# Kernel optimization log

Measured on AMD Instinct MI355X. Metric: run time of the kernel, lower is better.

Reference implementation:

```python
import jax, jax.numpy as jnp
import numpy as np

DIM = 1024
NUM_HEADS = 8
HEAD_DIM = 128
MAX_SEQ_LEN = 2048
ATTN_SCALE = 0.12
RMS_EPS = 1.1920929e-07  # torch float32 eps (F.rms_norm default)


def rms_norm(x):
    return x * jax.lax.rsqrt(jnp.mean(jnp.square(x), axis=-1, keepdims=True) + RMS_EPS)


def rope_tables(T):
    # angular_freq: (1/1024)**linspace(0,1,head_dim//4), padded with head_dim//4 zeros -> length head_dim//2
    af = (1.0 / 1024.0) ** np.linspace(0.0, 1.0, HEAD_DIM // 4, dtype=np.float32)
    af = np.concatenate([af, np.zeros(HEAD_DIM // 4, dtype=np.float32)])
    t = np.arange(T, dtype=np.float32)
    theta = np.einsum('i,j->ij', t, af)  # [T, head_dim//2]
    return jnp.asarray(np.cos(theta)), jnp.asarray(np.sin(theta))


def apply_rope(x_BTHD, cos, sin):
    # cos/sin: [T, head_dim//2] -> broadcast [1,T,1,hd//2]
    c = cos[None, :, None, :]
    s = sin[None, :, None, :]
    x1, x2 = jnp.split(x_BTHD, 2, axis=-1)
    y1 = x1 * c + x2 * s
    y2 = -x1 * s + x2 * c
    return jnp.concatenate([y1, y2], axis=-1)


def setup_inputs() -> dict:
    key = jax.random.key(0)
    k1, k2, k3, k4, k5 = jax.random.split(key, 5)
    B, T = 4, 2048
    hdim = NUM_HEADS * HEAD_DIM
    std = 0.5 * DIM ** (-0.5)
    bound = (3.0 ** 0.5) * std
    x = jax.random.normal(k1, (B, T, DIM), dtype=jnp.float32)
    ve = jax.random.normal(k2, (B, T, DIM), dtype=jnp.float32)
    sa_lambdas = jax.random.uniform(k3, (2,), dtype=jnp.float32)
    qkv_w = jax.random.uniform(k4, (3, hdim, DIM), dtype=jnp.float32, minval=-bound, maxval=bound)
    # original inits c_proj to zeros; use small random so the output is non-trivial
    c_proj_weight = jax.random.normal(k5, (DIM, hdim), dtype=jnp.float32) * 0.02
    return {"x": x, "ve": ve, "sa_lambdas": sa_lambdas, "qkv_w": qkv_w,
            "c_proj_weight": c_proj_weight}


def reference(x, ve, sa_lambdas, qkv_w, c_proj_weight):
    B, T, D = x.shape
    H, hd = NUM_HEADS, HEAD_DIM
    Wqkv = qkv_w.reshape(3 * H * hd, D)
    qkv = jnp.einsum('btd,ed->bte', x, Wqkv).reshape(B, T, 3 * H, hd)
    q, k, v = jnp.split(qkv, 3, axis=-2)  # each [B,T,H,hd]
    q, k = rms_norm(q), rms_norm(k)
    cos, sin = rope_tables(T)
    q, k = apply_rope(q, cos, sin), apply_rope(k, cos, sin)
    v = sa_lambdas[0] * v + sa_lambdas[1] * ve.reshape(B, T, H, hd)
    # [B,H,T,T] scores
    attn = jnp.einsum('bqhd,bkhd->bhqk', q, k) * ATTN_SCALE
    causal = jnp.triu(jnp.ones((T, T), dtype=bool), k=1)
    attn = jnp.where(causal[None, None], -jnp.inf, attn)
    attn = jax.nn.softmax(attn, axis=-1)
    y = jnp.einsum('bhqk,bkhd->bqhd', attn, v).reshape(B, T, H * hd)
    return jnp.einsum('bte,de->btd', y, c_proj_weight)
```

## Files before the change

kernel.cpp:

```cpp
#include <hip/hip_runtime.h>

#define DIM 1024
#define NH 8
#define HD 128
#define T_SEQ 2048
#define NTOK 8192
#define QKV_N 3072
#define ATTN_SCALE 0.12f
#define RMS_EPS 1.1920929e-07f

using f32x4  = __attribute__((ext_vector_type(4))) float;
using bf16x8 = __attribute__((ext_vector_type(8))) __bf16;

__device__ __forceinline__ unsigned short f2bf(float f) {
    unsigned int u = __builtin_bit_cast(unsigned int, f);
    u += 0x7fffu + ((u >> 16) & 1u);
    return (unsigned short)(u >> 16);
}
__device__ __forceinline__ float bf2f(unsigned short s) {
    unsigned int u = ((unsigned int)s) << 16;
    return __builtin_bit_cast(float, u);
}

__device__ __forceinline__ void gll16(const void* g, void* l) {
    __builtin_amdgcn_global_load_lds(
        (const __attribute__((address_space(1))) unsigned int*)g,
        (__attribute__((address_space(3))) unsigned int*)l, 16, 0, 0);
}

#define VMCNT(n) asm volatile("s_waitcnt vmcnt(" #n ")" ::: "memory")

__global__ __launch_bounds__(256) void cvt_f32_bf16(const float* __restrict__ in,
                                                    unsigned short* __restrict__ out,
                                                    int n4) {
    int i = blockIdx.x * 256 + threadIdx.x;
    if (i < n4) {
        float4 f = ((const float4*)in)[i];
        ushort4 o;
        o.x = f2bf(f.x); o.y = f2bf(f.y); o.z = f2bf(f.z); o.w = f2bf(f.w);
        ((ushort4*)out)[i] = o;
    }
}

#define GBM 256
#define GBN 128
#define GBK 64
#define SLOT_A 32768
#define SLOT_SZ 49152

template<int OUTF32>
__global__ __launch_bounds__(512, 1) void gemm256(const unsigned short* __restrict__ A,
                                                  const unsigned short* __restrict__ B,
                                                  void* __restrict__ Cout,
                                                  int M, int N, int K, int nbn) {
    __shared__ __align__(16) char smem[147456];
    const int tid  = threadIdx.x;
    const int lane = tid & 63;
    const int w    = tid >> 6;
    const int wm   = w >> 1, wn = w & 1;
    const int lr   = lane & 15, lg = lane >> 4;
    const int xsw  = (lr & 7) << 3;

    const int chunk = gridDim.x >> 3;
    const int bid2  = (blockIdx.x & 7) * chunk + (blockIdx.x >> 3);
    const int m0 = (bid2 / nbn) * GBM;
    const int n0 = (bid2 % nbn) * GBN;

    const int rsub = lane >> 3;
    const int csw  = ((lane & 7) ^ rsub) << 3;

    char* s0 = smem;
    char* s1 = smem + SLOT_SZ;
    char* s2 = smem + 2*SLOT_SZ;

    auto stage = [&](int kt, char* slot) {
        const int kb = kt * GBK;
        #pragma unroll
        for (int i = 0; i < 4; ++i) {
            int c = w*4 + i;
            gll16(&A[(size_t)(m0 + c*8 + rsub)*K + kb + csw], slot + c*1024);
        }
        #pragma unroll
        for (int i = 0; i < 2; ++i) {
            int c = w*2 + i;
            gll16(&B[(size_t)(n0 + c*8 + rsub)*K + kb + csw], slot + SLOT_A + c*1024);
        }
    };

    f32x4 acc[4][4] = {};
    const int KT = K / GBK;

    stage(0, s0);
    stage(1, s1);
    VMCNT(6);
    __builtin_amdgcn_s_barrier();
    __builtin_amdgcn_sched_barrier(0);

    for (int t = 0; t < KT; ++t) {
        if (t + 2 < KT) stage(t + 2, s2);
        const unsigned short* sA = (const unsigned short*)s0;
        const unsigned short* sB = (const unsigned short*)(s0 + SLOT_A);
        bf16x8 bfr[4][2];
        #pragma unroll
        for (int n = 0; n < 4; ++n)
            #pragma unroll
            for (int kk = 0; kk < 2; ++kk)
                bfr[n][kk] = *(const bf16x8*)&sB[(wn*64 + n*16 + lr)*64 + ((kk*32 + lg*8) ^ xsw)];
        #pragma unroll
        for (int m = 0; m < 4; ++m) {
            bf16x8 af[2];
            #pragma unroll
            for (int kk = 0; kk < 2; ++kk)
                af[kk] = *(const bf16x8*)&sA[(wm*64 + m*16 + lr)*64 + ((kk*32 + lg*8) ^ xsw)];
            __builtin_amdgcn_s_setprio(1);
            #pragma unroll
            for (int n = 0; n < 4; ++n)
                #pragma unroll
                for (int kk = 0; kk < 2; ++kk)
                    acc[m][n] = __builtin_amdgcn_mfma_f32_16x16x32_bf16(af[kk], bfr[n][kk], acc[m][n], 0, 0, 0);
            __builtin_amdgcn_s_setprio(0);
        }
        if (t + 2 < KT) { VMCNT(6); }
        else            { VMCNT(0); }
        __builtin_amdgcn_s_barrier();
        __builtin_amdgcn_sched_barrier(0);
        char* tmp = s0; s0 = s1; s1 = s2; s2 = tmp;
    }

    __syncthreads();
    float* sc = (float*)(smem + (size_t)w * 17408);
    #pragma unroll
    for (int m = 0; m < 4; ++m)
        #pragma unroll
        for (int n = 0; n < 4; ++n)
            #pragma unroll
            for (int r = 0; r < 4; ++r)
                sc[(m*16 + lg*4 + r)*68 + n*16 + lr] = acc[m][n][r];

    if (OUTF32) {
        float* C = (float*)Cout;
        #pragma unroll
        for (int rnd = 0; rnd < 16; ++rnd) {
            int g = rnd*64 + lane;
            int row = g >> 4, c4 = (g & 15) * 4;
            float4 v = *(float4*)&sc[row*68 + c4];
            *(float4*)&C[(size_t)(m0 + wm*64 + row)*N + n0 + wn*64 + c4] = v;
        }
    } else {
        unsigned short* C = (unsigned short*)Cout;
        #pragma unroll
        for (int rnd = 0; rnd < 8; ++rnd) {
            int g = rnd*64 + lane;
            int row = g >> 3, c8 = (g & 7) * 8;
            float4 v0 = *(float4*)&sc[row*68 + c8];
            float4 v1 = *(float4*)&sc[row*68 + c8 + 4];
            uint4 o;
            o.x = f2bf(v0.x) | ((unsigned)f2bf(v0.y) << 16);
            o.y = f2bf(v0.z) | ((unsigned)f2bf(v0.w) << 16);
            o.z = f2bf(v1.x) | ((unsigned)f2bf(v1.y) << 16);
            o.w = f2bf(v1.z) | ((unsigned)f2bf(v1.w) << 16);
            *(uint4*)&C[(size_t)(m0 + wm*64 + row)*N + n0 + wn*64 + c8] = o;
        }
    }
}

__global__ __launch_bounds__(256) void qkv_post(const unsigned short* __restrict__ qkv,
                                                unsigned short* __restrict__ qO,
                                                unsigned short* __restrict__ kO) {
    int gw   = (blockIdx.x * 256 + threadIdx.x) >> 6;
    int lane = threadIdx.x & 63;
    int h     = gw & 7;
    int token = gw >> 3;
    int t     = token & (T_SEQ-1);
    int b     = token >> 11;

    const unsigned short* base = qkv + (size_t)token * QKV_N + h*HD;
    float q1 = bf2f(base[lane]),        q2 = bf2f(base[lane+64]);
    float k1 = bf2f(base[1024+lane]),   k2 = bf2f(base[1024+lane+64]);

    float sq = q1*q1 + q2*q2;
    float sk = k1*k1 + k2*k2;
    #pragma unroll
    for (int m = 1; m < 64; m <<= 1) {
        sq += __shfl_xor(sq, m);
        sk += __shfl_xor(sk, m);
    }
    float qs = rsqrtf(sq * (1.0f/128.0f) + RMS_EPS) * ATTN_SCALE;
    float ks = rsqrtf(sk * (1.0f/128.0f) + RMS_EPS);
    q1 *= qs; q2 *= qs; k1 *= ks; k2 *= ks;

    float theta = (lane < 32) ? (float)t * exp2f((float)lane * (-10.0f/31.0f)) : 0.0f;
    float sn, cs;
    sincosf(theta, &sn, &cs);
    float qy1 =  q1*cs + q2*sn, qy2 = -q1*sn + q2*cs;
    float ky1 =  k1*cs + k2*sn, ky2 = -k1*sn + k2*cs;

    size_t obase = ((size_t)(b*NH + h) * T_SEQ + t) * HD;
    qO[obase + lane]      = f2bf(qy1);
    qO[obase + lane + 64] = f2bf(qy2);
    kO[obase + lane]      = f2bf(ky1);
    kO[obase + lane + 64] = f2bf(ky2);
}

__global__ __launch_bounds__(256) void vmix_t(const unsigned short* __restrict__ qkv,
                                              const float* __restrict__ ve,
                                              const float* __restrict__ lam,
                                              unsigned short* __restrict__ vt) {
    __shared__ unsigned short lT[128*72];
    const int tid = threadIdx.x;
    const int t0  = blockIdx.x * 64;
    const int bh  = blockIdx.y;
    const int b = bh >> 3, h = bh & 7;
    const float l0 = lam[0], l1 = lam[1];

    #pragma unroll
    for (int it = 0; it < 4; ++it) {
        int g  = it*256 + tid;
        int t  = g >> 4;
        int d8 = (g & 15) << 3;
        size_t token = (size_t)b*T_SEQ + t0 + t;
        ushort4 v0 = *(const ushort4*)&qkv[token*QKV_N + 2048 + h*HD + d8];
        ushort4 v1 = *(const ushort4*)&qkv[token*QKV_N + 2048 + h*HD + d8 + 4];
        float4 e0 = *(const float4*)&ve[token*DIM + h*HD + d8];
        float4 e1 = *(const float4*)&ve[token*DIM + h*HD + d8 + 4];
        lT[(d8+0)*72 + t] = f2bf(l0*bf2f(v0.x) + l1*e0.x);
        lT[(d8+1)*72 + t] = f2bf(l0*bf2f(v0.y) + l1*e0.y);
        lT[(d8+2)*72 + t] = f2bf(l0*bf2f(v0.z) + l1*e0.z);
        lT[(d8+3)*72 + t] = f2bf(l0*bf2f(v0.w) + l1*e0.w);
        lT[(d8+4)*72 + t] = f2bf(l0*bf2f(v1.x) + l1*e1.x);
        lT[(d8+5)*72 + t] = f2bf(l0*bf2f(v1.y) + l1*e1.y);
        lT[(d8+6)*72 + t] = f2bf(l0*bf2f(v1.z) + l1*e1.z);
        lT[(d8+7)*72 + t] = f2bf(l0*bf2f(v1.w) + l1*e1.w);
    }
    __syncthreads();
    #pragma unroll
    for (int it = 0; it < 4; ++it) {
        int g  = it*256 + tid;
        int d  = g >> 3;
        int t8 = (g & 7) << 3;
        uint4 pk = *(const uint4*)&lT[d*72 + t8];
        *(uint4*)&vt[((size_t)bh*HD + d)*T_SEQ + t0 + t8] = pk;
    }
}

__global__ __launch_bounds__(256) void attn_fwd(const unsigned short* __restrict__ Q,
                                                const unsigned short* __restrict__ K,
                                                const unsigned short* __restrict__ Vt,
                                                unsigned short* __restrict__ Y) {
    __shared__ unsigned short lK[2][64*128];
    __shared__ unsigned short lV[2][128*64];
    __shared__ unsigned short lP[4][16*64];

    const int tid  = threadIdx.x;
    const int lane = tid & 63;
    const int w    = tid >> 6;
    const int lr   = lane & 15, lg = lane >> 4;

    const int lin = blockIdx.y * 16 + blockIdx.x;
    const int bh  = (lin & 7)*4 + ((lin >> 3) & 3);
    const int p   = lin >> 5;
    const int qtA = p, qtB = 31 - p;

    const unsigned short* Qg = Q  + (size_t)bh * T_SEQ * HD;
    const unsigned short* Kg = K  + (size_t)bh * T_SEQ * HD;
    const unsigned short* Vg = Vt + (size_t)bh * HD * T_SEQ;
    const int q0A = qtA*64 + w*16;
    const int q0B = qtB*64 + w*16;

    auto stage = [&](int kt, int s) {
        const int kbase = kt * 64;
        #pragma unroll
        for (int i = 0; i < 4; ++i) {
            int c = w*4 + i;
            int row = c*4 + (lane >> 4);
            int col = ((lane & 15) << 3) ^ ((row & 7) << 3);
            gll16(&Kg[(size_t)(kbase + row)*HD + col], &lK[s][c*512]);
        }
        #pragma unroll
        for (int i = 0; i < 4; ++i) {
            int c = w*4 + i;
            int row = c*8 + (lane >> 3);
            int col = ((lane & 7) << 3) ^ ((row & 7) << 3);
            gll16(&Vg[(size_t)row*T_SEQ + kbase + col], &lV[s][c*512]);
        }
    };

    bf16x8 qfA[4], qfB[4];
    #pragma unroll
    for (int kk = 0; kk < 4; ++kk) {
        qfA[kk] = *(const bf16x8*)&Qg[(size_t)(q0A + lr)*HD + kk*32 + lg*8];
        qfB[kk] = *(const bf16x8*)&Qg[(size_t)(q0B + lr)*HD + kk*32 + lg*8];
    }
    VMCNT(0);
    #pragma unroll
    for (int kk = 0; kk < 4; ++kk)
        asm volatile("" :: "v"(qfA[kk]), "v"(qfB[kk]));

    f32x4 oA[8] = {}, oB[8] = {};
    float psA[4] = {0.f,0.f,0.f,0.f}, psB[4] = {0.f,0.f,0.f,0.f};

    auto pass = [&](const bf16x8* qf, f32x4* o, float* ps, int q0, bool diag,
                    int kbase, const unsigned short* lKc, const unsigned short* lVc) {
        f32x4 sf[4];
        #pragma unroll
        for (int j = 0; j < 4; ++j) {
            f32x4 s = {0.f,0.f,0.f,0.f};
            __builtin_amdgcn_s_setprio(1);
            #pragma unroll
            for (int kk = 0; kk < 4; ++kk) {
                bf16x8 kf = *(const bf16x8*)&lKc[(j*16+lr)*128 + ((kk*32 + lg*8) ^ ((lr&7)<<3))];
                s = __builtin_amdgcn_mfma_f32_16x16x32_bf16(qf[kk], kf, s, 0, 0, 0);
            }
            __builtin_amdgcn_s_setprio(0);
            sf[j] = s;
        }
        if (diag) {
            #pragma unroll
            for (int j = 0; j < 4; ++j)
                #pragma unroll
                for (int r = 0; r < 4; ++r) {
                    int kcol = kbase + j*16 + lr;
                    int qrow = q0 + lg*4 + r;
                    if (kcol > qrow) sf[j][r] = -INFINITY;
                }
        }
        #pragma unroll
        for (int j = 0; j < 4; ++j)
            #pragma unroll
            for (int r = 0; r < 4; ++r) {
                float pp = __expf(sf[j][r]);
                sf[j][r] = pp;
                ps[r] += pp;
            }
        #pragma unroll
        for (int j = 0; j < 4; ++j)
            #pragma unroll
            for (int r = 0; r < 4; ++r) {
                int prow = lg*4 + r;
                lP[w][prow*64 + ((j*16 + lr) ^ ((prow&7)<<3))] = f2bf(sf[j][r]);
            }
        asm volatile("" ::: "memory");
        bf16x8 pf[2];
        #pragma unroll
        for (int kk = 0; kk < 2; ++kk)
            pf[kk] = *(const bf16x8*)&lP[w][lr*64 + ((kk*32 + lg*8) ^ ((lr&7)<<3))];
        #pragma unroll
        for (int n = 0; n < 8; ++n) {
            __builtin_amdgcn_s_setprio(1);
            #pragma unroll
            for (int kk = 0; kk < 2; ++kk) {
                bf16x8 vf = *(const bf16x8*)&lVc[(n*16+lr)*64 + ((kk*32 + lg*8) ^ ((lr&7)<<3))];
                o[n] = __builtin_amdgcn_mfma_f32_16x16x32_bf16(pf[kk], vf, o[n], 0, 0, 0);
            }
            __builtin_amdgcn_s_setprio(0);
        }
    };

    stage(0, 0);
    for (int kt = 0; kt <= qtB; ++kt) {
        __builtin_amdgcn_s_barrier();
        const bool pre = (kt + 1 <= qtB);
        if (pre) stage(kt + 1, (kt + 1) & 1);
        if (pre) { VMCNT(8); }
        else     { VMCNT(0); }
        __builtin_amdgcn_sched_barrier(0);
        const int kbase = kt * 64;
        const unsigned short* lKc = lK[kt & 1];
        const unsigned short* lVc = lV[kt & 1];
        if (kt <= qtA) pass(qfA, oA, psA, q0A, kt == qtA, kbase, lKc, lVc);
        pass(qfB, oB, psB, q0B, kt == qtB, kbase, lKc, lVc);
    }

    #pragma unroll
    for (int m = 1; m < 16; m <<= 1)
        #pragma unroll
        for (int r = 0; r < 4; ++r) {
            psA[r] += __shfl_xor(psA[r], m);
            psB[r] += __shfl_xor(psB[r], m);
        }
    float riA[4], riB[4];
    #pragma unroll
    for (int r = 0; r < 4; ++r) { riA[r] = 1.0f / psA[r]; riB[r] = 1.0f / psB[r]; }

    const int b = bh >> 3, h = bh & 7;
    #pragma unroll
    for (int n = 0; n < 8; ++n)
        #pragma unroll
        for (int r = 0; r < 4; ++r) {
            int d = n*16 + lr;
            int qrowA = q0A + lg*4 + r;
            int qrowB = q0B + lg*4 + r;
            Y[((size_t)(b*T_SEQ + qrowA))*DIM + h*HD + d] = f2bf(oA[n][r] * riA[r]);
            Y[((size_t)(b*T_SEQ + qrowB))*DIM + h*HD + d] = f2bf(oB[n][r] * riB[r]);
        }
}

extern "C" void kernel_launch(void* const* d_in, const int* in_sizes, int n_in,
                              void* d_out, int out_size, void* d_ws, size_t ws_size,
                              hipStream_t stream) {
    const float* x      = (const float*)d_in[0];
    const float* ve     = (const float*)d_in[1];
    const float* lam    = (const float*)d_in[2];
    const float* qkvw   = (const float*)d_in[3];
    const float* cprojw = (const float*)d_in[4];

    char* ws = (char*)d_ws;
    unsigned short* xb  = (unsigned short*)(ws);
    unsigned short* wqb = (unsigned short*)(ws + 16777216);
    unsigned short* cpb = (unsigned short*)(ws + 23068672);
    unsigned short* qkv = (unsigned short*)(ws + 25165824);
    unsigned short* qa  = (unsigned short*)(ws + 75497472);
    unsigned short* ka  = (unsigned short*)(ws + 92274688);
    unsigned short* vt  = (unsigned short*)(ws + 109051904);
    unsigned short* ya  = (unsigned short*)(ws + 125829120);

    cvt_f32_bf16<<<8192, 256, 0, stream>>>(x, xb, 2097152);
    cvt_f32_bf16<<<3072, 256, 0, stream>>>(qkvw, wqb, 786432);
    cvt_f32_bf16<<<1024, 256, 0, stream>>>(cprojw, cpb, 262144);

    gemm256<0><<<768, 512, 0, stream>>>(xb, wqb, qkv, NTOK, QKV_N, DIM, 24);
    qkv_post<<<16384, 256, 0, stream>>>(qkv, qa, ka);
    vmix_t<<<dim3(32, 32), 256, 0, stream>>>(qkv, ve, lam, vt);
    attn_fwd<<<dim3(16, 32), 256, 0, stream>>>(qa, ka, vt, ya);
    gemm256<1><<<256, 512, 0, stream>>>(ya, cpb, (float*)d_out, NTOK, DIM, DIM, 8);
}
```

Baseline: 202.1 us.

## Add 256x256 eight-phase QKV GEMM, RoPE table, fused dual-tile attention pass

Adds a new 256x256-tile GEMM with an eight-wave phased schedule (split LDS halves, barriers between MFMA phases) for the QKV projection, which halves the grid and increases operand reuse per tile. The attention kernel now shares each K fragment and each V fragment between both query tiles in one combined pass, and switches to exp2 with log2e folded into the q scale. RoPE cos/sin are precomputed into a table in the workspace rather than computed with sincos per thread. Attention gets a launch bound hint of 2 blocks per CU. These trade higher register pressure and heavier barrier synchronisation for fewer LDS reads and less transcendental work.

```diff
diff --git a/kernel.cpp b/kernel.cpp
--- a/kernel.cpp
+++ b/kernel.cpp
@@ -29,6 +29,9 @@
 }
 
 #define VMCNT(n) asm volatile("s_waitcnt vmcnt(" #n ")" ::: "memory")
+#define LGKM0 do { asm volatile("s_waitcnt lgkmcnt(0)" ::: "memory"); \
+                   __builtin_amdgcn_sched_barrier(0); } while(0)
+#define PH_BAR __builtin_amdgcn_s_barrier()
 
 __global__ __launch_bounds__(256) void cvt_f32_bf16(const float* __restrict__ in,
                                                     unsigned short* __restrict__ out,
@@ -42,9 +45,189 @@
     }
 }
 
-#define GBM 256
-#define GBN 128
-#define GBK 64
+__global__ __launch_bounds__(256) void rope_tab(float2* __restrict__ tab) {
+    int idx = blockIdx.x * 256 + threadIdx.x;
+    int t = idx >> 5, i = idx & 31;
+    float th = (float)t * exp2f((float)i * (-10.0f/31.0f));
+    float sn, cs;
+    sincosf(th, &sn, &cs);
+    tab[idx] = make_float2(cs, sn);
+}
+
+template<int OUTF32>
+__global__ __launch_bounds__(512, 1) void gemm8p(const unsigned short* __restrict__ A,
+                                                 const unsigned short* __restrict__ B,
+                                                 void* __restrict__ Cout,
+                                                 int M, int N, int K, int nbn) {
+    __shared__ __align__(16) char smem[139264];
+    const int tid  = threadIdx.x;
+    const int lane = tid & 63;
+    const int w    = tid >> 6;
+    const int wm   = w >> 2, wn = w & 3;
+    const int lr   = lane & 15, lg = lane >> 4;
+
+    const int chunk = gridDim.x >> 3;
+    const int bid2  = (blockIdx.x & 7) * chunk + (blockIdx.x >> 3);
+    const int bm = (bid2 / nbn) * 256;
+    const int bn = (bid2 % nbn) * 256;
+
+    const int srow = lane >> 3;
+    const int scol = ((lane & 7) ^ srow) << 3;
+    const int KT = K / 64;
+
+    auto ldsA = [&](int p, int h) -> unsigned short* {
+        return (unsigned short*)(smem + p*65536 + h*16384);
+    };
+    auto ldsB = [&](int p, int h) -> unsigned short* {
+        return (unsigned short*)(smem + p*65536 + 32768 + h*16384);
+    };
+    auto stA = [&](int t, int p, int h) {
+        if (t >= KT) return;
+        char* dst = (char*)ldsA(p, h);
+        #pragma unroll
+        for (int i = 0; i < 2; ++i) {
+            int c = w*2 + i;
+            gll16(&A[(size_t)(bm + h*128 + c*8 + srow)*K + t*64 + scol], dst + c*1024);
+        }
+    };
+    auto stB = [&](int t, int p, int h) {
+        if (t >= KT) return;
+        char* dst = (char*)ldsB(p, h);
+        #pragma unroll
+        for (int i = 0; i < 2; ++i) {
+            int c = w*2 + i;
+            gll16(&B[(size_t)(bn + h*128 + c*8 + srow)*K + t*64 + scol], dst + c*1024);
+        }
+    };
+
+    f32x4 acc[8][4] = {};
+    bf16x8 a[4][2], b0[2][2], b1[2][2];
+
+    auto rdA4 = [&](int p, int qm) {
+        const unsigned short* base = ldsA(p, wm);
+        #pragma unroll
+        for (int m = 0; m < 4; ++m) {
+            int row = qm*64 + m*16 + lr;
+            int sw = (row & 7) << 3;
+            #pragma unroll
+            for (int kk = 0; kk < 2; ++kk)
+                a[m][kk] = *(const bf16x8*)&base[row*64 + ((kk*32 + lg*8) ^ sw)];
+        }
+    };
+    auto rdB2 = [&](int p, int qn, bf16x8 (*bq)[2]) {
+        const unsigned short* base = ldsB(p, wn >> 1);
+        #pragma unroll
+        for (int n = 0; n < 2; ++n) {
+            int row = (wn & 1)*64 + qn*32 + n*16 + lr;
+            int sw = (row & 7) << 3;
+            #pragma unroll
+            for (int kk = 0; kk < 2; ++kk)
+                bq[n][kk] = *(const bf16x8*)&base[row*64 + ((kk*32 + lg*8) ^ sw)];
+        }
+    };
+    auto mm = [&](int qm, int qn, bf16x8 (*bq)[2]) {
+        __builtin_amdgcn_s_setprio(1);
+        #pragma unroll
+        for (int m = 0; m < 4; ++m)
+            #pragma unroll
+            for (int n = 0; n < 2; ++n)
+                #pragma unroll
+                for (int kk = 0; kk < 2; ++kk)
+                    acc[qm*4+m][qn*2+n] =
+                        __builtin_amdgcn_mfma_f32_16x16x32_bf16(a[m][kk], bq[n][kk],
+                                                                acc[qm*4+m][qn*2+n], 0, 0, 0);
+        __builtin_amdgcn_s_setprio(0);
+    };
+
+    stB(0, 0, 0); stB(0, 0, 1); stA(0, 0, 0); stA(0, 0, 1);
+    stB(1, 1, 0); stB(1, 1, 1);
+    VMCNT(4);
+    PH_BAR;
+
+    for (int i = 0; i < KT/2; ++i) {
+        const int t0 = 2*i;
+        const bool steady = (i + 1 < KT/2);
+        rdA4(0, 0); rdB2(0, 0, b0);
+        stA(t0+1, 1, 0);
+        PH_BAR; LGKM0;
+        mm(0, 0, b0);
+        PH_BAR;
+        rdB2(0, 1, b1);
+        stA(t0+1, 1, 1);
+        PH_BAR; LGKM0;
+        mm(0, 1, b1);
+        PH_BAR;
+        rdA4(0, 1);
+        stB(t0+2, 0, 0);
+        PH_BAR; LGKM0;
+        mm(1, 0, b0);
+        PH_BAR;
+        stB(t0+2, 0, 1);
+        if (steady) { VMCNT(4); } else { VMCNT(0); }
+        PH_BAR;
+        mm(1, 1, b1);
+        PH_BAR;
+        rdA4(1, 0); rdB2(1, 0, b0);
+        stA(t0+2, 0, 0);
+        PH_BAR; LGKM0;
+        mm(0, 0, b0);
+        PH_BAR;
+        rdB2(1, 1, b1);
+        stA(t0+2, 0, 1);
+        PH_BAR; LGKM0;
+        mm(0, 1, b1);
+        PH_BAR;
+        rdA4(1, 1);
+        stB(t0+3, 1, 0);
+        PH_BAR; LGKM0;
+        mm(1, 0, b0);
+        PH_BAR;
+        stB(t0+3, 1, 1);
+        if (steady) { VMCNT(4); } else { VMCNT(0); }
+        PH_BAR;
+        mm(1, 1, b1);
+        PH_BAR;
+    }
+
+    __syncthreads();
+    float* sc = (float*)(smem + (size_t)w * 17408);
+    #pragma unroll
+    for (int f = 0; f < 2; ++f) {
+        #pragma unroll
+        for (int m = 0; m < 4; ++m)
+            #pragma unroll
+            for (int n = 0; n < 4; ++n)
+                #pragma unroll
+                for (int r = 0; r < 4; ++r)
+                    sc[(m*16 + lg*4 + r)*68 + n*16 + lr] = acc[f*4+m][n][r];
+        if (OUTF32) {
+            float* C = (float*)Cout;
+            #pragma unroll
+            for (int rnd = 0; rnd < 16; ++rnd) {
+                int g = rnd*64 + lane;
+                int row = g >> 4, c4 = (g & 15) * 4;
+                float4 v = *(float4*)&sc[row*68 + c4];
+                *(float4*)&C[(size_t)(bm + wm*128 + f*64 + row)*N + bn + wn*64 + c4] = v;
+            }
+        } else {
+            unsigned short* C = (unsigned short*)Cout;
+            #pragma unroll
+            for (int rnd = 0; rnd < 8; ++rnd) {
+                int g = rnd*64 + lane;
+                int row = g >> 3, c8 = (g & 7) * 8;
+                float4 v0 = *(float4*)&sc[row*68 + c8];
+                float4 v1 = *(float4*)&sc[row*68 + c8 + 4];
+                uint4 o;
+                o.x = f2bf(v0.x) | ((unsigned)f2bf(v0.y) << 16);
+                o.y = f2bf(v0.z) | ((unsigned)f2bf(v0.w) << 16);
+                o.z = f2bf(v1.x) | ((unsigned)f2bf(v1.y) << 16);
+                o.w = f2bf(v1.z) | ((unsigned)f2bf(v1.w) << 16);
+                *(uint4*)&C[(size_t)(bm + wm*128 + f*64 + row)*N + bn + wn*64 + c8] = o;
+            }
+        }
+    }
+}
+
 #define SLOT_A 32768
 #define SLOT_SZ 49152
 
@@ -63,8 +246,8 @@
 
     const int chunk = gridDim.x >> 3;
     const int bid2  = (blockIdx.x & 7) * chunk + (blockIdx.x >> 3);
-    const int m0 = (bid2 / nbn) * GBM;
-    const int n0 = (bid2 % nbn) * GBN;
+    const int m0 = (bid2 / nbn) * 256;
+    const int n0 = (bid2 % nbn) * 128;
 
     const int rsub = lane >> 3;
     const int csw  = ((lane & 7) ^ rsub) << 3;
@@ -74,7 +257,7 @@
     char* s2 = smem + 2*SLOT_SZ;
 
     auto stage = [&](int kt, char* slot) {
-        const int kb = kt * GBK;
+        const int kb = kt * 64;
         #pragma unroll
         for (int i = 0; i < 4; ++i) {
             int c = w*4 + i;
@@ -88,7 +271,7 @@
     };
 
     f32x4 acc[4][4] = {};
-    const int KT = K / GBK;
+    const int KT = K / 64;
 
     stage(0, s0);
     stage(1, s1);
@@ -165,6 +348,7 @@
 }
 
 __global__ __launch_bounds__(256) void qkv_post(const unsigned short* __restrict__ qkv,
+                                                const float2* __restrict__ tab,
                                                 unsigned short* __restrict__ qO,
                                                 unsigned short* __restrict__ kO) {
     int gw   = (blockIdx.x * 256 + threadIdx.x) >> 6;
@@ -185,13 +369,12 @@
         sq += __shfl_xor(sq, m);
         sk += __shfl_xor(sk, m);
     }
-    float qs = rsqrtf(sq * (1.0f/128.0f) + RMS_EPS) * ATTN_SCALE;
+    float qs = rsqrtf(sq * (1.0f/128.0f) + RMS_EPS) * (ATTN_SCALE * 1.44269504088896f);
     float ks = rsqrtf(sk * (1.0f/128.0f) + RMS_EPS);
     q1 *= qs; q2 *= qs; k1 *= ks; k2 *= ks;
 
-    float theta = (lane < 32) ? (float)t * exp2f((float)lane * (-10.0f/31.0f)) : 0.0f;
-    float sn, cs;
-    sincosf(theta, &sn, &cs);
+    float cs = 1.0f, sn = 0.0f;
+    if (lane < 32) { float2 cc = tab[t*32 + lane]; cs = cc.x; sn = cc.y; }
     float qy1 =  q1*cs + q2*sn, qy2 = -q1*sn + q2*cs;
     float ky1 =  k1*cs + k2*sn, ky2 = -k1*sn + k2*cs;
 
@@ -243,10 +426,10 @@
     }
 }
 
-__global__ __launch_bounds__(256) void attn_fwd(const unsigned short* __restrict__ Q,
-                                                const unsigned short* __restrict__ K,
-                                                const unsigned short* __restrict__ Vt,
-                                                unsigned short* __restrict__ Y) {
+__global__ __launch_bounds__(256, 2) void attn_fwd(const unsigned short* __restrict__ Q,
+                                                   const unsigned short* __restrict__ K,
+                                                   const unsigned short* __restrict__ Vt,
+                                                   unsigned short* __restrict__ Y) {
     __shared__ unsigned short lK[2][64*128];
     __shared__ unsigned short lV[2][128*64];
     __shared__ unsigned short lP[4][16*64];
@@ -299,28 +482,109 @@
     f32x4 oA[8] = {}, oB[8] = {};
     float psA[4] = {0.f,0.f,0.f,0.f}, psB[4] = {0.f,0.f,0.f,0.f};
 
-    auto pass = [&](const bf16x8* qf, f32x4* o, float* ps, int q0, bool diag,
-                    int kbase, const unsigned short* lKc, const unsigned short* lVc) {
-        f32x4 sf[4];
+    auto passAB = [&](bool diagA, int kbase,
+                      const unsigned short* lKc, const unsigned short* lVc) {
+        f32x4 sfA[4], sfB[4];
+        __builtin_amdgcn_s_setprio(1);
         #pragma unroll
         for (int j = 0; j < 4; ++j) {
-            f32x4 s = {0.f,0.f,0.f,0.f};
-            __builtin_amdgcn_s_setprio(1);
+            f32x4 sA = {0.f,0.f,0.f,0.f}, sB = {0.f,0.f,0.f,0.f};
             #pragma unroll
             for (int kk = 0; kk < 4; ++kk) {
                 bf16x8 kf = *(const bf16x8*)&lKc[(j*16+lr)*128 + ((kk*32 + lg*8) ^ ((lr&7)<<3))];
-                s = __builtin_amdgcn_mfma_f32_16x16x32_bf16(qf[kk], kf, s, 0, 0, 0);
-            }
-            __builtin_amdgcn_s_setprio(0);
-            sf[j] = s;
-        }
-        if (diag) {
+                sA = __builtin_amdgcn_mfma_f32_16x16x32_bf16(qfA[kk], kf, sA, 0, 0, 0);
+                sB = __builtin_amdgcn_mfma_f32_16x16x32_bf16(qfB[kk], kf, sB, 0, 0, 0);
+            }
+            sfA[j] = sA; sfB[j] = sB;
+        }
+        __builtin_amdgcn_s_setprio(0);
+        if (diagA) {
             #pragma unroll
             for (int j = 0; j < 4; ++j)
                 #pragma unroll
                 for (int r = 0; r < 4; ++r) {
                     int kcol = kbase + j*16 + lr;
-                    int qrow = q0 + lg*4 + r;
+                    int qrow = q0A + lg*4 + r;
+                    if (kcol > qrow) sfA[j][r] = -INFINITY;
+                }
+        }
+        #pragma unroll
+        for (int j = 0; j < 4; ++j)
+            #pragma unroll
+            for (int r = 0; r < 4; ++r) {
+                float pp = exp2f(sfA[j][r]);
+                sfA[j][r] = pp;
+                psA[r] += pp;
+            }
+        asm volatile("" ::: "memory");
+        #pragma unroll
+        for (int j = 0; j < 4; ++j)
+            #pragma unroll
+            for (int r = 0; r < 4; ++r) {
+                int prow = lg*4 + r;
+                lP[w][prow*64 + ((j*16 + lr) ^ ((prow&7)<<3))] = f2bf(sfA[j][r]);
+            }
+        asm volatile("" ::: "memory");
+        bf16x8 pfA[2];
+        #pragma unroll
+        for (int kk = 0; kk < 2; ++kk)
+            pfA[kk] = *(const bf16x8*)&lP[w][lr*64 + ((kk*32 + lg*8) ^ ((lr&7)<<3))];
+        #pragma unroll
+        for (int j = 0; j < 4; ++j)
+            #pragma unroll
+            for (int r = 0; r < 4; ++r) {
+                float pp = exp2f(sfB[j][r]);
+                sfB[j][r] = pp;
+                psB[r] += pp;
+            }
+        asm volatile("" ::: "memory");
+        #pragma unroll
+        for (int j = 0; j < 4; ++j)
+            #pragma unroll
+            for (int r = 0; r < 4; ++r) {
+                int prow = lg*4 + r;
+                lP[w][prow*64 + ((j*16 + lr) ^ ((prow&7)<<3))] = f2bf(sfB[j][r]);
+            }
+        asm volatile("" ::: "memory");
+        bf16x8 pfB[2];
+        #pragma unroll
+        for (int kk = 0; kk < 2; ++kk)
+            pfB[kk] = *(const bf16x8*)&lP[w][lr*64 + ((kk*32 + lg*8) ^ ((lr&7)<<3))];
+        #pragma unroll
+        for (int n = 0; n < 8; ++n) {
+            bf16x8 vf0 = *(const bf16x8*)&lVc[(n*16+lr)*64 + (( 0 + lg*8) ^ ((lr&7)<<3))];
+            bf16x8 vf1 = *(const bf16x8*)&lVc[(n*16+lr)*64 + ((32 + lg*8) ^ ((lr&7)<<3))];
+            __builtin_amdgcn_s_setprio(1);
+            oA[n] = __builtin_amdgcn_mfma_f32_16x16x32_bf16(pfA[0], vf0, oA[n], 0, 0, 0);
+            oA[n] = __builtin_amdgcn_mfma_f32_16x16x32_bf16(pfA[1], vf1, oA[n], 0, 0, 0);
+            oB[n] = __builtin_amdgcn_mfma_f32_16x16x32_bf16(pfB[0], vf0, oB[n], 0, 0, 0);
+            oB[n] = __builtin_amdgcn_mfma_f32_16x16x32_bf16(pfB[1], vf1, oB[n], 0, 0, 0);
+            __builtin_amdgcn_s_setprio(0);
+        }
+    };
+
+    auto pass = [&](bool diag, int kbase,
+                    const unsigned short* lKc, const unsigned short* lVc) {
+        f32x4 sf[4];
+        __builtin_amdgcn_s_setprio(1);
+        #pragma unroll
+        for (int j = 0; j < 4; ++j) {
+            f32x4 s = {0.f,0.f,0.f,0.f};
+            #pragma unroll
+            for (int kk = 0; kk < 4; ++kk) {
+                bf16x8 kf = *(const bf16x8*)&lKc[(j*16+lr)*128 + ((kk*32 + lg*8) ^ ((lr&7)<<3))];
+                s = __builtin_amdgcn_mfma_f32_16x16x32_bf16(qfB[kk], kf, s, 0, 0, 0);
+            }
+            sf[j] = s;
+        }
+        __builtin_amdgcn_s_setprio(0);
+        if (diag) {
+            #pragma unroll
+            for (int j = 0; j < 4; ++j)
+                #pragma unroll
+                for (int r = 0; r < 4; ++r) {
+                    int kcol = kbase + j*16 + lr;
+                    int qrow = q0B + lg*4 + r;
                     if (kcol > qrow) sf[j][r] = -INFINITY;
                 }
         }
@@ -328,10 +592,11 @@
         for (int j = 0; j < 4; ++j)
             #pragma unroll
             for (int r = 0; r < 4; ++r) {
-                float pp = __expf(sf[j][r]);
+                float pp = exp2f(sf[j][r]);
                 sf[j][r] = pp;
-                ps[r] += pp;
-            }
+                psB[r] += pp;
+            }
+        asm volatile("" ::: "memory");
         #pragma unroll
         for (int j = 0; j < 4; ++j)
             #pragma unroll
@@ -346,12 +611,11 @@
             pf[kk] = *(const bf16x8*)&lP[w][lr*64 + ((kk*32 + lg*8) ^ ((lr&7)<<3))];
         #pragma unroll
         for (int n = 0; n < 8; ++n) {
+            bf16x8 vf0 = *(const bf16x8*)&lVc[(n*16+lr)*64 + (( 0 + lg*8) ^ ((lr&7)<<3))];
+            bf16x8 vf1 = *(const bf16x8*)&lVc[(n*16+lr)*64 + ((32 + lg*8) ^ ((lr&7)<<3))];
             __builtin_amdgcn_s_setprio(1);
-            #pragma unroll
-            for (int kk = 0; kk < 2; ++kk) {
-                bf16x8 vf = *(const bf16x8*)&lVc[(n*16+lr)*64 + ((kk*32 + lg*8) ^ ((lr&7)<<3))];
-                o[n] = __builtin_amdgcn_mfma_f32_16x16x32_bf16(pf[kk], vf, o[n], 0, 0, 0);
-            }
+            oB[n] = __builtin_amdgcn_mfma_f32_16x16x32_bf16(pf[0], vf0, oB[n], 0, 0, 0);
+            oB[n] = __builtin_amdgcn_mfma_f32_16x16x32_bf16(pf[1], vf1, oB[n], 0, 0, 0);
             __builtin_amdgcn_s_setprio(0);
         }
     };
@@ -361,14 +625,13 @@
         __builtin_amdgcn_s_barrier();
         const bool pre = (kt + 1 <= qtB);
         if (pre) stage(kt + 1, (kt + 1) & 1);
-        if (pre) { VMCNT(8); }
-        else     { VMCNT(0); }
+        if (pre) { VMCNT(8); } else { VMCNT(0); }
         __builtin_amdgcn_sched_barrier(0);
         const int kbase = kt * 64;
         const unsigned short* lKc = lK[kt & 1];
         const unsigned short* lVc = lV[kt & 1];
-        if (kt <= qtA) pass(qfA, oA, psA, q0A, kt == qtA, kbase, lKc, lVc);
-        pass(qfB, oB, psB, q0B, kt == qtB, kbase, lKc, lVc);
+        if (kt <= qtA) passAB(kt == qtA, kbase, lKc, lVc);
+        else           pass(kt == qtB, kbase, lKc, lVc);
     }
 
     #pragma unroll
@@ -413,13 +676,15 @@
     unsigned short* ka  = (unsigned short*)(ws + 92274688);
     unsigned short* vt  = (unsigned short*)(ws + 109051904);
     unsigned short* ya  = (unsigned short*)(ws + 125829120);
+    float2* tab = (float2*)(ws);
 
     cvt_f32_bf16<<<8192, 256, 0, stream>>>(x, xb, 2097152);
     cvt_f32_bf16<<<3072, 256, 0, stream>>>(qkvw, wqb, 786432);
     cvt_f32_bf16<<<1024, 256, 0, stream>>>(cprojw, cpb, 262144);
 
-    gemm256<0><<<768, 512, 0, stream>>>(xb, wqb, qkv, NTOK, QKV_N, DIM, 24);
-    qkv_post<<<16384, 256, 0, stream>>>(qkv, qa, ka);
+    gemm8p<0><<<384, 512, 0, stream>>>(xb, wqb, qkv, NTOK, QKV_N, DIM, 12);
+    rope_tab<<<256, 256, 0, stream>>>(tab);
+    qkv_post<<<16384, 256, 0, stream>>>(qkv, tab, qa, ka);
     vmix_t<<<dim3(32, 32), 256, 0, stream>>>(qkv, ve, lam, vt);
     attn_fwd<<<dim3(16, 32), 256, 0, stream>>>(qa, ka, vt, ya);
     gemm256<1><<<256, 512, 0, stream>>>(ya, cpb, (float*)d_out, NTOK, DIM, DIM, 8);
```

Result: no change. 203.9 us (+0.9%).
